# Performance work log

Hardware: AMD Instinct MI355X
Metric: run time of the kernel (lower is better)

The kernel has to match this reference:

```python
import jax, jax.numpy as jnp
import numpy as np
from jax import lax

WINDOW_SIZE = 11
SIGMA = 1.5
DATA_RANGE = 1.0


def _gaussian_window(channels):
    coords = jnp.arange(WINDOW_SIZE, dtype=jnp.float32) - WINDOW_SIZE // 2
    g = jnp.exp(-coords ** 2 / (2.0 * SIGMA ** 2))
    g = g / g.sum()
    w2d = jnp.outer(g, g)
    w2d = w2d / w2d.sum()
    # depthwise kernel: (C, 1, K, K) in OIHW with feature_group_count=C
    return jnp.broadcast_to(w2d, (channels, 1, WINDOW_SIZE, WINDOW_SIZE))


def _dwconv(x, window, channels):
    pad = WINDOW_SIZE // 2
    return lax.conv_general_dilated(
        x, window,
        window_strides=(1, 1),
        padding=[(pad, pad), (pad, pad)],
        dimension_numbers=('NCHW', 'OIHW', 'NCHW'),
        feature_group_count=channels,
    )


def setup_inputs() -> dict:
    key = jax.random.key(0)
    k1, k2 = jax.random.split(key)
    B, C, H, W = 16, 3, 512, 512
    x = jax.random.uniform(k1, (B, C, H, W), dtype=jnp.float32)
    y = jax.random.uniform(k2, (B, C, H, W), dtype=jnp.float32)
    return {"x": x, "y": y}


def reference(x, y):
    channels = x.shape[1]
    window = _gaussian_window(channels)
    mu_x = _dwconv(x, window, channels)
    mu_y = _dwconv(y, window, channels)
    mu_x2 = mu_x * mu_x
    mu_y2 = mu_y * mu_y
    mu_xy = mu_x * mu_y
    sigma_x2 = _dwconv(x * x, window, channels) - mu_x2
    sigma_y2 = _dwconv(y * y, window, channels) - mu_y2
    sigma_xy = _dwconv(x * y, window, channels) - mu_xy
    c1 = (0.01 * DATA_RANGE) ** 2
    c2 = (0.03 * DATA_RANGE) ** 2
    ssim_map = (2 * mu_xy + c1) * (2 * sigma_xy + c2) / (
        (mu_x2 + mu_y2 + c1) * (sigma_x2 + sigma_y2 + c2) + 1e-08)
    per_image = ssim_map.mean(axis=(1, 2, 3))
    return 1.0 - per_image.mean()
```

## Files before the change

kernel.cpp:

```cpp
#include <hip/hip_runtime.h>
#include <math.h>


#define IMG_W 512
#define IMG_H 512
#define PLANES 48
#define TX 64
#define TYS 128
#define RAD 5
#define NT 256
#define GDX (IMG_W / TX)
#define GDY (IMG_H / TYS)
#define NBLK (GDX * GDY * PLANES)
#define NCH 9
#define NCV 8
#define CSTRH 56
#define PSTRH 3584
#define NUMREC (IMG_W * IMG_H * 4)
#define CHSTEP (16 * IMG_W * 4)
#define INVW  0.26601181f
#define GC2   0.32059890f

typedef _Float16 h2 __attribute__((ext_vector_type(2)));
typedef _Float16 h4 __attribute__((ext_vector_type(4)));
typedef _Float16 h8 __attribute__((ext_vector_type(8)));
typedef float f32x4 __attribute__((ext_vector_type(4)));
typedef int i32x4 __attribute__((ext_vector_type(4)));

__device__ f32x4 buf_ld_x4(i32x4 srsrc, int voffset, int soffset, int aux)
    __asm("llvm.amdgcn.raw.buffer.load.v4f32");

__device__ __forceinline__ i32x4 make_srd(const float* p) {
    union { i32x4 v; struct { const float* p; unsigned rng; unsigned cfg; } s; } u;
    u.s.p = p; u.s.rng = NUMREC; u.s.cfg = 0x00020000u;
    return u.v;
}

__device__ __forceinline__ float exp2_fast(float a) {
#if __has_builtin(__builtin_amdgcn_exp2f)
    return __builtin_amdgcn_exp2f(a);
#else
    return exp2f(a);
#endif
}

__device__ __forceinline__ float wbandf(int idx) {
    const float fd = (float)(idx - 5);
    const float g = exp2_fast(-(fd * fd) * GC2) * INVW;
    return ((unsigned)idx <= 10u) ? g : 0.f;
}

__device__ __forceinline__ h2 pkrtz(float a, float b) {
    auto t = __builtin_amdgcn_cvt_pkrtz(a, b);
    h2 r;
    __builtin_memcpy(&r, &t, sizeof(r));
    return r;
}

__device__ __forceinline__ h4 pack4(f32x4 a) {
    const h2 lo = pkrtz(a[0], a[1]), hi = pkrtz(a[2], a[3]);
    h4 v;
    v[0] = lo.x; v[1] = lo.y; v[2] = hi.x; v[3] = hi.y;
    return v;
}

__device__ __forceinline__ void hconv_chunk(
    f32x4 xa, f32x4 xb, f32x4 ya, f32x4 yb, h8 whB,
    _Float16* wp)
{
    const f32x4 zz = {0.f, 0.f, 0.f, 0.f};
    const h2 xh0 = pkrtz(xa[0], xa[1]), xh1 = pkrtz(xa[2], xa[3]);
    const h2 xh2 = pkrtz(xb[0], xb[1]), xh3 = pkrtz(xb[2], xb[3]);
    const h2 yh0 = pkrtz(ya[0], ya[1]), yh1 = pkrtz(ya[2], ya[3]);
    const h2 yh2 = pkrtz(yb[0], yb[1]), yh3 = pkrtz(yb[2], yb[3]);
    const h2 s0 = xh0 + yh0, s1 = xh1 + yh1, s2 = xh2 + yh2, s3 = xh3 + yh3;
    const h2 d0 = xh0 - yh0, d1 = xh1 - yh1, d2 = xh2 - yh2, d3 = xh3 - yh3;
    h8 sA, dA;
    sA[0] = s0.x; sA[1] = s0.y; sA[2] = s1.x; sA[3] = s1.y;
    sA[4] = s2.x; sA[5] = s2.y; sA[6] = s3.x; sA[7] = s3.y;
    dA[0] = d0.x; dA[1] = d0.y; dA[2] = d1.x; dA[3] = d1.y;
    dA[4] = d2.x; dA[5] = d2.y; dA[6] = d3.x; dA[7] = d3.y;
    const h8 s2A = sA * sA;
    const h8 d2A = dA * dA;
    const f32x4 hS  = __builtin_amdgcn_mfma_f32_16x16x32_f16(sA,  whB, zz, 0, 0, 0);
    const f32x4 hD  = __builtin_amdgcn_mfma_f32_16x16x32_f16(dA,  whB, zz, 0, 0, 0);
    const f32x4 hS2 = __builtin_amdgcn_mfma_f32_16x16x32_f16(s2A, whB, zz, 0, 0, 0);
    const f32x4 hD2 = __builtin_amdgcn_mfma_f32_16x16x32_f16(d2A, whB, zz, 0, 0, 0);
    *(h4*)(wp + 0 * PSTRH) = pack4(hS);
    *(h4*)(wp + 1 * PSTRH) = pack4(hD);
    *(h4*)(wp + 2 * PSTRH) = pack4(hS2);
    *(h4*)(wp + 3 * PSTRH) = pack4(hD2);
}

__global__ __launch_bounds__(NT, 4) void ssim_tile_kernel(
    const float* __restrict__ x, const float* __restrict__ y,
    float* __restrict__ partials)
{
    __shared__ __align__(16) _Float16 Ht[4 * TX * CSTRH];
    __shared__ float wave_sums[NT / 64];

    const int tid = threadIdx.x;
    const int l = tid & 63, wid = tid >> 6;
    const int q = l >> 4, fc = l & 15;
    const int qh = q >> 1, ql = q & 1;

    const int plane = blockIdx.z;
    const i32x4 srdx = make_srd(x + (size_t)plane * IMG_H * IMG_W);
    const i32x4 srdy = make_srd(y + (size_t)plane * IMG_H * IMG_W);
    const int C0 = blockIdx.x * TX;
    const int R0 = blockIdx.y * TYS;
    const int c0 = 16 * wid;
    const int col = c0 + fc;
    const int gcol = C0 + c0 - 8 + 8 * q;
    const int gr0 = R0 - RAD + fc;
    int voff = ((unsigned)gcol < (unsigned)IMG_W)
             ? ((gr0 << 11) + (gcol << 2)) : 0x60000000;

    f32x4 LXA[3], LXB[3], LYA[3], LYB[3];
    #pragma unroll
    for (int c = 0; c < 3; ++c) {
        LXA[c] = buf_ld_x4(srdx, voff, 0, 0);
        LXB[c] = buf_ld_x4(srdx, voff, 16, 0);
        LYA[c] = buf_ld_x4(srdy, voff, 0, 0);
        LYB[c] = buf_ld_x4(srdy, voff, 16, 0);
        voff += CHSTEP;
    }

    float s2w = 0.f;
    #pragma unroll
    for (int k = 0; k <= 10; ++k) s2w += (float)(_Float16)wbandf(k);
    const float cv = 1.f / (s2w * s2w);

    h8 whB, wvA;
    #pragma unroll
    for (int e = 0; e < 8; ++e) whB[e] = (_Float16)wbandf(8 * q + e - fc - 3);
    #pragma unroll
    for (int e = 0; e < 5; ++e) wvA[e] = whB[e + 3];
    #pragma unroll
    for (int e = 5; e < 8; ++e) wvA[e] = (_Float16)wbandf(8 * q + e - fc);

    _Float16* const hw = Ht + col * CSTRH + 4 * q;
    const int rb = col * CSTRH + 8 * ql;

    hconv_chunk(LXA[0], LXB[0], LYA[0], LYB[0], whB, hw + 0 * 16);
    hconv_chunk(LXA[1], LXB[1], LYA[1], LYB[1], whB, hw + 1 * 16);

    const f32x4 zz = {0.f, 0.f, 0.f, 0.f};
    float local = 0.f;
    int vslot = qh;
    #pragma unroll
    for (int m = 0; m < NCV; ++m) {
        if (m + 3 < NCH) {
            LXA[m % 3] = buf_ld_x4(srdx, voff, 0, 0);
            LXB[m % 3] = buf_ld_x4(srdx, voff, 16, 0);
            LYA[m % 3] = buf_ld_x4(srdy, voff, 0, 0);
            LYB[m % 3] = buf_ld_x4(srdy, voff, 16, 0);
            voff += CHSTEP;
        }

        const _Float16* rp = Ht + rb + vslot * 16;
        const f32x4 aS  = __builtin_amdgcn_mfma_f32_16x16x32_f16(
            wvA, *(const h8*)(rp + 0 * PSTRH), zz, 0, 0, 0);
        const f32x4 aD  = __builtin_amdgcn_mfma_f32_16x16x32_f16(
            wvA, *(const h8*)(rp + 1 * PSTRH), zz, 0, 0, 0);
        const f32x4 aS2 = __builtin_amdgcn_mfma_f32_16x16x32_f16(
            wvA, *(const h8*)(rp + 2 * PSTRH), zz, 0, 0, 0);
        const f32x4 aD2 = __builtin_amdgcn_mfma_f32_16x16x32_f16(
            wvA, *(const h8*)(rp + 3 * PSTRH), zz, 0, 0, 0);
        vslot = (vslot == 2) ? 0 : vslot + 1;

        #pragma unroll
        for (int r = 0; r < 4; ++r) {
            const float mS = aS[r]  * cv, mD = aD[r]  * cv;
            const float eS = aS2[r] * cv, eD = aD2[r] * cv;
            const float ms2 = mS * mS, md2 = mD * mD;
            const float Pm = 0.5f * (ms2 - md2);
            const float Qm = 0.5f * (ms2 + md2);
            const float Pe = 0.5f * (eS - eD);
            const float Qe = 0.5f * (eS + eD);
            const float c1 = 1e-4f, c2 = 9e-4f;
            const float num = (Pm + c1) * (Pe - Pm + c2);
            const float den = (Qm + c1) * (Qe - Qm + c2) + 1e-8f;
            local += num * __builtin_amdgcn_rcpf(den);
        }

        if (m + 2 < NCH)
            hconv_chunk(LXA[(m + 2) % 3], LXB[(m + 2) % 3],
                        LYA[(m + 2) % 3], LYB[(m + 2) % 3],
                        whB, hw + ((m + 2) % 3) * 16);
    }

    #pragma unroll
    for (int off = 32; off > 0; off >>= 1)
        local += __shfl_down(local, off, 64);
    if (l == 0) wave_sums[wid] = local;
    __syncthreads();
    if (tid == 0) {
        const float s = wave_sums[0] + wave_sums[1] + wave_sums[2] + wave_sums[3];
        const int bid = blockIdx.x + GDX * (blockIdx.y + GDY * blockIdx.z);
        partials[bid] = s;
    }
}

__global__ __launch_bounds__(NT) void ssim_finalize_kernel(
    const float* __restrict__ partials, float* __restrict__ out)
{
    const int tid = threadIdx.x;
    double s = 0.0;
    #pragma unroll 4
    for (int i = tid; i < NBLK; i += NT) s += (double)partials[i];
    #pragma unroll
    for (int off = 32; off > 0; off >>= 1)
        s += __shfl_down(s, off, 64);
    __shared__ double ws_[NT / 64];
    const int lane = tid & 63, wv = tid >> 6;
    if (lane == 0) ws_[wv] = s;
    __syncthreads();
    if (tid == 0) {
        const double t = ws_[0] + ws_[1] + ws_[2] + ws_[3];
        const double n = (double)PLANES * IMG_H * IMG_W;
        out[0] = (float)(1.0 - t / n);
    }
}

extern "C" void kernel_launch(void* const* d_in, const int* in_sizes, int n_in,
                              void* d_out, int out_size, void* d_ws, size_t ws_size,
                              hipStream_t stream)
{
    const float* x = (const float*)d_in[0];
    const float* y = (const float*)d_in[1];
    float* out = (float*)d_out;
    float* partials = (float*)d_ws;

    dim3 grid(GDX, GDY, PLANES);
    ssim_tile_kernel<<<grid, NT, 0, stream>>>(x, y, partials);
    ssim_finalize_kernel<<<1, NT, 0, stream>>>(partials, out);
}
```

Before: 132.9 us.

## Split vertical conv into two accumulating MFMAs with single-slot LDS staging

The row tile is halved, so the grid gets twice as many blocks. The vertical pass is restructured so each 16-row output chunk is built from two MFMAs that accumulate across consecutive horizontal chunks, using split weight vectors wvA1 and wvA2. Because of this the LDS staging buffer only holds one 16-row slot instead of a three-slot ring, which cuts shared memory and allows higher occupancy (launch bounds 4 to 5). It also adds sched_barriers. Halving the tile raises halo overhead: 80 loaded rows per 64 output rows versus 144 per 128. The single-slot reuse also relies on wave-local ordering of LDS writes and reads.

```diff
diff --git a/kernel.cpp b/kernel.cpp
--- a/kernel.cpp
+++ b/kernel.cpp
@@ -6,16 +6,15 @@
 #define IMG_H 512
 #define PLANES 48
 #define TX 64
-#define TYS 128
+#define TYS 64
 #define RAD 5
 #define NT 256
 #define GDX (IMG_W / TX)
 #define GDY (IMG_H / TYS)
 #define NBLK (GDX * GDY * PLANES)
-#define NCH 9
-#define NCV 8
-#define CSTRH 56
-#define PSTRH 3584
+#define NCH 5
+#define CSTR 24
+#define PSTR (TX * CSTR)
 #define NUMREC (IMG_W * IMG_H * 4)
 #define CHSTEP (16 * IMG_W * 4)
 #define INVW  0.26601181f
@@ -86,23 +85,60 @@
     const f32x4 hD  = __builtin_amdgcn_mfma_f32_16x16x32_f16(dA,  whB, zz, 0, 0, 0);
     const f32x4 hS2 = __builtin_amdgcn_mfma_f32_16x16x32_f16(s2A, whB, zz, 0, 0, 0);
     const f32x4 hD2 = __builtin_amdgcn_mfma_f32_16x16x32_f16(d2A, whB, zz, 0, 0, 0);
-    *(h4*)(wp + 0 * PSTRH) = pack4(hS);
-    *(h4*)(wp + 1 * PSTRH) = pack4(hD);
-    *(h4*)(wp + 2 * PSTRH) = pack4(hS2);
-    *(h4*)(wp + 3 * PSTRH) = pack4(hD2);
-}
-
-__global__ __launch_bounds__(NT, 4) void ssim_tile_kernel(
+    *(h4*)(wp + 0 * PSTR) = pack4(hS);
+    *(h4*)(wp + 1 * PSTR) = pack4(hD);
+    *(h4*)(wp + 2 * PSTR) = pack4(hS2);
+    *(h4*)(wp + 3 * PSTR) = pack4(hD2);
+}
+
+__device__ __forceinline__ float mapsum(f32x4 aS, f32x4 aD, f32x4 aS2, f32x4 aD2,
+                                        float cv)
+{
+    float local = 0.f;
+    #pragma unroll
+    for (int r = 0; r < 4; ++r) {
+        const float mS = aS[r]  * cv, mD = aD[r]  * cv;
+        const float eS = aS2[r] * cv, eD = aD2[r] * cv;
+        const float ms2 = mS * mS, md2 = mD * mD;
+        const float Pm = 0.5f * (ms2 - md2);
+        const float Qm = 0.5f * (ms2 + md2);
+        const float Pe = 0.5f * (eS - eD);
+        const float Qe = 0.5f * (eS + eD);
+        const float c1 = 1e-4f, c2 = 9e-4f;
+        const float num = (Pm + c1) * (Pe - Pm + c2);
+        const float den = (Qm + c1) * (Qe - Qm + c2) + 1e-8f;
+        local += num * __builtin_amdgcn_rcpf(den);
+    }
+    return local;
+}
+
+#define MFMA16(A, B, C) __builtin_amdgcn_mfma_f32_16x16x32_f16((A), (B), (C), 0, 0, 0)
+
+#define VSTART(ACC) do {                         \
+    ACC[0] = MFMA16(wvA1, B0, zz);               \
+    ACC[1] = MFMA16(wvA1, B1, zz);               \
+    ACC[2] = MFMA16(wvA1, B2, zz);               \
+    ACC[3] = MFMA16(wvA1, B3, zz);               \
+} while (0)
+
+#define VFINISH(ACC) do {                        \
+    const f32x4 fS  = MFMA16(wvA2, B0, ACC[0]);  \
+    const f32x4 fD  = MFMA16(wvA2, B1, ACC[1]);  \
+    const f32x4 fS2 = MFMA16(wvA2, B2, ACC[2]);  \
+    const f32x4 fD2 = MFMA16(wvA2, B3, ACC[3]);  \
+    local += mapsum(fS, fD, fS2, fD2, cv);       \
+} while (0)
+
+__global__ __launch_bounds__(NT, 5) void ssim_tile_kernel(
     const float* __restrict__ x, const float* __restrict__ y,
     float* __restrict__ partials)
 {
-    __shared__ __align__(16) _Float16 Ht[4 * TX * CSTRH];
+    __shared__ __align__(16) _Float16 Ht[4 * PSTR];
     __shared__ float wave_sums[NT / 64];
 
     const int tid = threadIdx.x;
     const int l = tid & 63, wid = tid >> 6;
     const int q = l >> 4, fc = l & 15;
-    const int qh = q >> 1, ql = q & 1;
 
     const int plane = blockIdx.z;
     const i32x4 srdx = make_srd(x + (size_t)plane * IMG_H * IMG_W);
@@ -116,78 +152,70 @@
     int voff = ((unsigned)gcol < (unsigned)IMG_W)
              ? ((gr0 << 11) + (gcol << 2)) : 0x60000000;
 
-    f32x4 LXA[3], LXB[3], LYA[3], LYB[3];
-    #pragma unroll
-    for (int c = 0; c < 3; ++c) {
-        LXA[c] = buf_ld_x4(srdx, voff, 0, 0);
-        LXB[c] = buf_ld_x4(srdx, voff, 16, 0);
-        LYA[c] = buf_ld_x4(srdy, voff, 0, 0);
-        LYB[c] = buf_ld_x4(srdy, voff, 16, 0);
+    f32x4 LXA[2], LXB[2], LYA[2], LYB[2];
+    #pragma unroll
+    for (int cpl = 0; cpl < 2; ++cpl) {
+        LXA[cpl] = buf_ld_x4(srdx, voff, 0, 0);
+        LXB[cpl] = buf_ld_x4(srdx, voff, 16, 0);
+        LYA[cpl] = buf_ld_x4(srdy, voff, 0, 0);
+        LYB[cpl] = buf_ld_x4(srdy, voff, 16, 0);
         voff += CHSTEP;
     }
+    __builtin_amdgcn_sched_barrier(0);
 
     float s2w = 0.f;
     #pragma unroll
     for (int k = 0; k <= 10; ++k) s2w += (float)(_Float16)wbandf(k);
     const float cv = 1.f / (s2w * s2w);
 
-    h8 whB, wvA;
-    #pragma unroll
-    for (int e = 0; e < 8; ++e) whB[e] = (_Float16)wbandf(8 * q + e - fc - 3);
-    #pragma unroll
-    for (int e = 0; e < 5; ++e) wvA[e] = whB[e + 3];
-    #pragma unroll
-    for (int e = 5; e < 8; ++e) wvA[e] = (_Float16)wbandf(8 * q + e - fc);
-
-    _Float16* const hw = Ht + col * CSTRH + 4 * q;
-    const int rb = col * CSTRH + 8 * ql;
-
-    hconv_chunk(LXA[0], LXB[0], LYA[0], LYB[0], whB, hw + 0 * 16);
-    hconv_chunk(LXA[1], LXB[1], LYA[1], LYB[1], whB, hw + 1 * 16);
-
+    h8 whB, wvA1, wvA2;
+    #pragma unroll
+    for (int e = 0; e < 8; ++e) {
+        const int k = 8 * q + e;
+        whB[e]  = (_Float16)wbandf(k - fc - 3);
+        wvA1[e] = (_Float16)((k < 16) ? wbandf(k - fc)      : 0.f);
+        wvA2[e] = (_Float16)((k < 16) ? wbandf(k + 16 - fc) : 0.f);
+    }
+
+    _Float16* const hw = Ht + col * CSTR + 4 * q;
+    const _Float16* const rbase = Ht + col * CSTR + 8 * (q & 1);
+
+    f32x4 acc0[4], acc1[4];
     const f32x4 zz = {0.f, 0.f, 0.f, 0.f};
     float local = 0.f;
-    int vslot = qh;
-    #pragma unroll
-    for (int m = 0; m < NCV; ++m) {
-        if (m + 3 < NCH) {
-            LXA[m % 3] = buf_ld_x4(srdx, voff, 0, 0);
-            LXB[m % 3] = buf_ld_x4(srdx, voff, 16, 0);
-            LYA[m % 3] = buf_ld_x4(srdy, voff, 0, 0);
-            LYB[m % 3] = buf_ld_x4(srdy, voff, 16, 0);
+
+    #pragma unroll
+    for (int c = 0; c < NCH; ++c) {
+        if (c >= 1) {
+            const h8 B0 = *(const h8*)(rbase + 0 * PSTR);
+            const h8 B1 = *(const h8*)(rbase + 1 * PSTR);
+            const h8 B2 = *(const h8*)(rbase + 2 * PSTR);
+            const h8 B3 = *(const h8*)(rbase + 3 * PSTR);
+            if (c & 1) {
+                if (c >= 2) VFINISH(acc1);
+                VSTART(acc0);
+            } else {
+                if (c >= 2) VFINISH(acc0);
+                VSTART(acc1);
+            }
+        }
+        hconv_chunk(LXA[c & 1], LXB[c & 1], LYA[c & 1], LYB[c & 1], whB, hw);
+        if (c + 2 < NCH) {
+            LXA[c & 1] = buf_ld_x4(srdx, voff, 0, 0);
+            LXB[c & 1] = buf_ld_x4(srdx, voff, 16, 0);
+            LYA[c & 1] = buf_ld_x4(srdy, voff, 0, 0);
+            LYB[c & 1] = buf_ld_x4(srdy, voff, 16, 0);
             voff += CHSTEP;
         }
-
-        const _Float16* rp = Ht + rb + vslot * 16;
-        const f32x4 aS  = __builtin_amdgcn_mfma_f32_16x16x32_f16(
-            wvA, *(const h8*)(rp + 0 * PSTRH), zz, 0, 0, 0);
-        const f32x4 aD  = __builtin_amdgcn_mfma_f32_16x16x32_f16(
-            wvA, *(const h8*)(rp + 1 * PSTRH), zz, 0, 0, 0);
-        const f32x4 aS2 = __builtin_amdgcn_mfma_f32_16x16x32_f16(
-            wvA, *(const h8*)(rp + 2 * PSTRH), zz, 0, 0, 0);
-        const f32x4 aD2 = __builtin_amdgcn_mfma_f32_16x16x32_f16(
-            wvA, *(const h8*)(rp + 3 * PSTRH), zz, 0, 0, 0);
-        vslot = (vslot == 2) ? 0 : vslot + 1;
-
-        #pragma unroll
-        for (int r = 0; r < 4; ++r) {
-            const float mS = aS[r]  * cv, mD = aD[r]  * cv;
-            const float eS = aS2[r] * cv, eD = aD2[r] * cv;
-            const float ms2 = mS * mS, md2 = mD * mD;
-            const float Pm = 0.5f * (ms2 - md2);
-            const float Qm = 0.5f * (ms2 + md2);
-            const float Pe = 0.5f * (eS - eD);
-            const float Qe = 0.5f * (eS + eD);
-            const float c1 = 1e-4f, c2 = 9e-4f;
-            const float num = (Pm + c1) * (Pe - Pm + c2);
-            const float den = (Qm + c1) * (Qe - Qm + c2) + 1e-8f;
-            local += num * __builtin_amdgcn_rcpf(den);
-        }
-
-        if (m + 2 < NCH)
-            hconv_chunk(LXA[(m + 2) % 3], LXB[(m + 2) % 3],
-                        LYA[(m + 2) % 3], LYB[(m + 2) % 3],
-                        whB, hw + ((m + 2) % 3) * 16);
+        __builtin_amdgcn_sched_barrier(0);
+    }
+
+    {
+        const h8 B0 = *(const h8*)(rbase + 0 * PSTR);
+        const h8 B1 = *(const h8*)(rbase + 1 * PSTR);
+        const h8 B2 = *(const h8*)(rbase + 2 * PSTR);
+        const h8 B3 = *(const h8*)(rbase + 3 * PSTR);
+        VFINISH(acc1);
     }
 
     #pragma unroll
```

Measured after the change: 135.3 us. Within noise of the previous version (+1.8%).
